# Optimization experiments

Measured on AMD Instinct MI355X. Metric: run time of the kernel, lower is better.

The kernel has to match this reference:

```python
import jax, jax.numpy as jnp
import numpy as np

LOG_SIG_MIN, LOG_SIG_MAX = -20.0, 2.0
N_NODES, N_EDGES, B = 16384, 131072, 256
NF, EF, GF, H, A = 64, 32, 16, 256, 8


def seg_mean(x, idx, num):
    # segment mean with empty-segment protection
    s = jax.ops.segment_sum(x, idx, num_segments=num)
    c = jax.ops.segment_sum(jnp.ones((x.shape[0], 1), x.dtype), idx, num_segments=num)
    return s / jnp.maximum(c, 1.0)


def setup_inputs() -> dict:
    key = jax.random.key(0)
    ks = jax.random.split(key, 32)
    def xav(k, i, o):
        lim = np.sqrt(6.0 / (i + o)).astype(np.float32)
        return jax.random.uniform(k, (i, o), jnp.float32, -lim, lim)
    inp = {
        'node_feats': jax.random.normal(ks[0], (N_NODES, NF), jnp.float32),
        'edge_feats': jax.random.normal(ks[1], (N_EDGES, EF), jnp.float32),
        'global_feats': jax.random.normal(ks[2], (B, GF), jnp.float32),
        'receivers': jax.random.randint(ks[3], (N_EDGES,), 0, N_NODES, jnp.int32),
        'node_graph': jnp.sort(jax.random.randint(ks[4], (N_NODES,), 0, B, jnp.int32)),
        'edge_graph': jnp.sort(jax.random.randint(ks[5], (N_EDGES,), 0, B, jnp.int32)),
        # edge1: edge_features only -> 256
        'We1': xav(ks[6], EF, 256), 'be1': jnp.zeros((256,), jnp.float32),
        # node1: node_features + aggregated incoming edges (256) -> 256
        'Wn1': xav(ks[7], NF, 256), 'Win1': xav(ks[8], 256, 256), 'bn1': jnp.zeros((256,), jnp.float32),
        # edge2: edge_features(256) + global(16) -> 128
        'We2': xav(ks[9], 256, 128), 'Weg2': xav(ks[10], GF, 128), 'be2': jnp.zeros((128,), jnp.float32),
        # node2: node(256) + incoming edges(128) + global(16) -> 128
        'Wn2': xav(ks[11], 256, 128), 'Win2': xav(ks[12], 128, 128), 'Wng2': xav(ks[13], GF, 128), 'bn2': jnp.zeros((128,), jnp.float32),
        # global: avg nodes(128) + avg edges(128) + global(16) -> H
        'Ugn': xav(ks[14], 128, H), 'Uge': xav(ks[15], 128, H), 'Ugg': xav(ks[16], GF, H), 'bg': jnp.zeros((H,), jnp.float32),
        # heads
        'Wm': xav(ks[17], H, A), 'bm': jnp.zeros((A,), jnp.float32),
        'Ws': xav(ks[18], H, A), 'bs': jnp.zeros((A,), jnp.float32),
    }
    return inp


def reference(node_feats, edge_feats, global_feats, receivers, node_graph, edge_graph,
              We1, be1, Wn1, Win1, bn1, We2, Weg2, be2, Wn2, Win2, Wng2, bn2,
              Ugn, Uge, Ugg, bg, Wm, bm, Ws, bs):
    # edge block 1: [N_EDGES, 256]
    e1 = jax.nn.relu(edge_feats @ We1 + be1)
    # node block 1: node linear + mean of incoming edges
    n1 = jax.nn.relu(node_feats @ Wn1 + seg_mean(e1, receivers, N_NODES) @ Win1 + bn1)
    # edge block 2: edge + per-graph global (gather)
    e2 = jax.nn.relu(e1 @ We2 + global_feats[edge_graph] @ Weg2 + be2)
    # node block 2
    n2 = jax.nn.relu(n1 @ Wn2 + seg_mean(e2, receivers, N_NODES) @ Win2 + global_feats[node_graph] @ Wng2 + bn2)
    # global block: per-graph mean over nodes and edges (scatter-reduce)
    u = seg_mean(n2, node_graph, B) @ Ugn + seg_mean(e2, edge_graph, B) @ Uge + global_feats @ Ugg + bg
    g = jax.nn.relu(u)
    mean = g @ Wm + bm
    log_std = jnp.clip(g @ Ws + bs, LOG_SIG_MIN, LOG_SIG_MAX)
    return mean, log_std
```

## Files before the change

kernel.cpp:

```cpp
#include <hip/hip_runtime.h>
#include <cstddef>

#define N_NODES 16384
#define N_EDGES 131072
#define BGR 256
#define NF 64
#define EF 32
#define GF 16

typedef __attribute__((ext_vector_type(8))) short bf16x8;
typedef __attribute__((ext_vector_type(4))) float f32x4;

#define MFMA16(a, b, c) __builtin_amdgcn_mfma_f32_16x16x32_bf16((a), (b), (c), 0, 0, 0)
__device__ const f32x4 ZERO4 = {0.f, 0.f, 0.f, 0.f};

__device__ inline unsigned short f2bf(float f) {
    return (unsigned short)((__builtin_bit_cast(unsigned, f) + 0x8000u) >> 16);
}
__device__ inline float bfs(short x) {
    return __builtin_bit_cast(float, (unsigned)((unsigned short)x) << 16);
}

__device__ inline bf16x8 pack8(float4 f0, float4 f1) {
    bf16x8 a;
    a[0] = (short)f2bf(f0.x); a[1] = (short)f2bf(f0.y);
    a[2] = (short)f2bf(f0.z); a[3] = (short)f2bf(f0.w);
    a[4] = (short)f2bf(f1.x); a[5] = (short)f2bf(f1.y);
    a[6] = (short)f2bf(f1.z); a[7] = (short)f2bf(f1.w);
    return a;
}

extern "C" __global__ void __launch_bounds__(256)
k_prep(const float* __restrict__ We1, const float* __restrict__ We2,
       const float* __restrict__ Wn1, const float* __restrict__ Win1,
       const float* __restrict__ Wn2, const float* __restrict__ Win2,
       unsigned short* We1p, unsigned short* We2p, unsigned short* Wn1p,
       unsigned short* Win1p, unsigned short* Wn2p, unsigned short* Win2p,
       const float* __restrict__ gf,
       const float* __restrict__ Weg2, const float* __restrict__ be2,
       const float* __restrict__ Wng2, const float* __restrict__ bn2,
       float* __restrict__ gproj_e, float* __restrict__ gproj_n,
       const int* __restrict__ receivers, int* cntR,
       const int* __restrict__ node_graph, const int* __restrict__ edge_graph,
       int* offN, int* offE)
{
    const int bid = blockIdx.x, tid = threadIdx.x;
    if (bid < 84) {
        const int fi = bid * 4 + (tid >> 6), l = tid & 63;
        const float* W; unsigned short* P; int N, t;
        if      (fi < 16)  { W = We1;  P = We1p;  N = 256; t = fi;       }
        else if (fi < 80)  { W = We2;  P = We2p;  N = 128; t = fi - 16;  }
        else if (fi < 112) { W = Wn1;  P = Wn1p;  N = 256; t = fi - 80;  }
        else if (fi < 240) { W = Win1; P = Win1p; N = 256; t = fi - 112; }
        else if (fi < 304) { W = Wn2;  P = Wn2p;  N = 128; t = fi - 240; }
        else               { W = Win2; P = Win2p; N = 128; t = fi - 304; }
        const int NT = N / 16;
        const int kt = t / NT, nt = t % NT;
        const int k0 = kt * 32 + (l >> 4) * 8;
        const int col = nt * 16 + (l & 15);
        unsigned short* dst = P + ((size_t)t * 64 + l) * 8;
        #pragma unroll
        for (int j = 0; j < 8; ++j) dst[j] = f2bf(W[(size_t)(k0 + j) * N + col]);
    } else if (bid < 212) {
        const int b = (bid - 84) * 2 + (tid >> 7), t = tid & 127;
        float ge = be2[t], gn = bn2[t];
        #pragma unroll
        for (int j = 0; j < GF; ++j) {
            const float g = gf[b * GF + j];
            ge = fmaf(g, Weg2[j * 128 + t], ge);
            gn = fmaf(g, Wng2[j * 128 + t], gn);
        }
        gproj_e[b * 128 + t] = ge;
        gproj_n[b * 128 + t] = gn;
    } else if (bid < 724) {
        const int i = (bid - 212) * 256 + tid;
        atomicAdd(&cntR[receivers[i]], 1);
    } else {
        const int g = tid;
        const int* arr = (bid == 725) ? edge_graph : node_graph;
        int* dst       = (bid == 725) ? offE       : offN;
        const int len  = (bid == 725) ? N_EDGES    : N_NODES;
        int lo = 0, hi = len;
        while (lo < hi) {
            const int mid = (lo + hi) >> 1;
            if (arr[mid] < g) lo = mid + 1; else hi = mid;
        }
        dst[g] = lo;
        if (g == 0) dst[256] = len;
    }
}

extern "C" __global__ void __launch_bounds__(256)
k_scanA(const int* __restrict__ cntR, int* __restrict__ offR, int* __restrict__ bsum)
{
    __shared__ int sm[256];
    const int b = blockIdx.x, t = threadIdx.x;
    const int4 v = *(const int4*)(cntR + b * 1024 + t * 4);
    const int s = v.x + v.y + v.z + v.w;
    sm[t] = s; __syncthreads();
    for (int o = 1; o < 256; o <<= 1) {
        int x = (t >= o) ? sm[t - o] : 0;
        __syncthreads(); sm[t] += x; __syncthreads();
    }
    const int excl = sm[t] - s;
    int4 o;
    o.x = excl; o.y = excl + v.x; o.z = o.y + v.y; o.w = o.z + v.z;
    *(int4*)(offR + b * 1024 + t * 4) = o;
    if (t == 255) bsum[b] = sm[255];
}

extern "C" __global__ void __launch_bounds__(256)
k_scanB(int* __restrict__ offR, const int* __restrict__ bsum)
{
    const int i = blockIdx.x * 256 + threadIdx.x;
    if (i > 16384) return;
    const int g = i >> 10;
    int pre = 0;
    for (int k = 0; k < g; ++k) pre += bsum[k];
    offR[i] = (i < 16384 ? offR[i] : 0) + pre;
}

extern "C" __global__ void __launch_bounds__(256)
k_scatter(const int* __restrict__ receivers, const int* __restrict__ offR,
          int* curR, int* perm)
{
    const int i = blockIdx.x * 256 + threadIdx.x;
    if (i < N_EDGES) {
        const int r = receivers[i];
        const int pos = offR[r] + atomicAdd(&curR[r], 1);
        perm[pos] = i;
    }
}

extern "C" __global__ void __launch_bounds__(256)
k_edge(const float* __restrict__ edge_feats,
       const int* __restrict__ perm,
       const int* __restrict__ edge_graph,
       const unsigned short* __restrict__ We1p,
       const unsigned short* __restrict__ We2p,
       const float* __restrict__ be1,
       const float* __restrict__ gproj_e,
       unsigned short* __restrict__ e1p,
       unsigned short* __restrict__ e2p,
       unsigned short* __restrict__ e2g)
{
    __shared__ __align__(16) unsigned short e1s[64 * 256];
    const int tid = threadIdx.x;
    const int w = tid >> 6, l = tid & 63;
    const int lr = l & 15, lq = l >> 4;
    const int e0 = blockIdx.x * 64;
    char* B = (char*)e1s;

    int eidA[4];
    int egC[4][4];
    #pragma unroll
    for (int g = 0; g < 4; ++g) eidA[g] = perm[e0 + g * 16 + lr];
    #pragma unroll
    for (int g = 0; g < 4; ++g)
        #pragma unroll
        for (int i = 0; i < 4; ++i)
            egC[g][i] = edge_graph[perm[e0 + g * 16 + lq * 4 + i]];

    bf16x8 a[4];
    #pragma unroll
    for (int g = 0; g < 4; ++g) {
        const float* s = edge_feats + (size_t)eidA[g] * EF + lq * 8;
        a[g] = pack8(*(const float4*)s, *(const float4*)(s + 4));
    }
    #pragma unroll
    for (int j = 0; j < 4; ++j) {
        const int nt = w * 4 + j;
        bf16x8 bfr = *(const bf16x8*)(We1p + ((size_t)nt * 64 + l) * 8);
        const int col = nt * 16 + lr;
        const float bias = be1[col];
        #pragma unroll
        for (int g = 0; g < 4; ++g) {
            f32x4 c = MFMA16(a[g], bfr, ZERO4);
            #pragma unroll
            for (int i = 0; i < 4; ++i) {
                const int row = g * 16 + lq * 4 + i;
                const float v = fmaxf(c[i] + bias, 0.f);
                *(unsigned short*)(B + row * 512 + ((col * 2) ^ ((row & 7) << 4))) = f2bf(v);
            }
        }
    }
    __syncthreads();

    #pragma unroll
    for (int it = 0; it < 8; ++it) {
        const int flat = it * 4096 + tid * 16;
        const int row = flat >> 9, colb = flat & 511;
        bf16x8 v = *(const bf16x8*)(B + row * 512 + (colb ^ ((row & 7) << 4)));
        *(bf16x8*)(e1p + (size_t)(e0 + row) * 256 + (colb >> 1)) = v;
    }

    f32x4 acc[4][2];
    #pragma unroll
    for (int g = 0; g < 4; ++g) {
        acc[g][0] = ZERO4;
        acc[g][1] = ZERO4;
    }
    #pragma unroll
    for (int kt = 0; kt < 8; ++kt) {
        bf16x8 pA[4];
        #pragma unroll
        for (int g = 0; g < 4; ++g) {
            const int row = g * 16 + lr;
            pA[g] = *(const bf16x8*)(B + row * 512 + ((kt * 64 + lq * 16) ^ ((lr & 7) << 4)));
        }
        #pragma unroll
        for (int j = 0; j < 2; ++j) {
            const int nt = w * 2 + j;
            bf16x8 bfr = *(const bf16x8*)(We2p + ((size_t)(kt * 8 + nt) * 64 + l) * 8);
            #pragma unroll
            for (int g = 0; g < 4; ++g) acc[g][j] = MFMA16(pA[g], bfr, acc[g][j]);
        }
    }
    __syncthreads();

    #pragma unroll
    for (int j = 0; j < 2; ++j) {
        const int nt = w * 2 + j, col = nt * 16 + lr;
        #pragma unroll
        for (int g = 0; g < 4; ++g)
            #pragma unroll
            for (int i = 0; i < 4; ++i) {
                const int row = g * 16 + lq * 4 + i;
                const float v = fmaxf(acc[g][j][i] + gproj_e[(size_t)egC[g][i] * 128 + col], 0.f);
                *(unsigned short*)(B + row * 512 + ((col * 2) ^ ((row & 7) << 4))) = f2bf(v);
            }
    }
    __syncthreads();
    #pragma unroll
    for (int it = 0; it < 4; ++it) {
        const int flat = it * 4096 + tid * 16;
        const int row = flat >> 8, colb = flat & 255;
        bf16x8 v = *(const bf16x8*)(B + row * 512 + (colb ^ ((row & 7) << 4)));
        const int eid = perm[e0 + row];
        *(bf16x8*)(e2p + (size_t)(e0 + row) * 128 + (colb >> 1)) = v;
        *(bf16x8*)(e2g + (size_t)eid * 128 + (colb >> 1)) = v;
    }
}

extern "C" __global__ void __launch_bounds__(256)
k_nodeagg(const float* __restrict__ node_feats,
          const int* __restrict__ node_graph,
          const int* __restrict__ offR,
          const unsigned short* __restrict__ e1p,
          const unsigned short* __restrict__ e2p,
          const unsigned short* __restrict__ Wn1p,
          const unsigned short* __restrict__ Win1p,
          const unsigned short* __restrict__ Wn2p,
          const unsigned short* __restrict__ Win2p,
          const float* __restrict__ bn1,
          const float* __restrict__ gproj_n,
          unsigned short* __restrict__ n2g)
{
    __shared__ __align__(16) unsigned short m1s[16 * 256];
    __shared__ __align__(16) unsigned short m2s[16 * 128];
    __shared__ __align__(16) unsigned short n1s[16 * 256];
    const int tid = threadIdx.x;
    const int w = tid >> 6, l = tid & 63;
    const int lr = l & 15, lq = l >> 4;
    const int n0 = blockIdx.x * 16;
    char* M1 = (char*)m1s; char* M2 = (char*)m2s; char* N1 = (char*)n1s;

    const int half = l >> 5, li = l & 31, q = l >> 4;
    for (int jn = 0; jn < 4; ++jn) {
        const int rn = w * 4 + jn, n = n0 + rn;
        const int c0 = offR[n], c1 = offR[n + 1];
        float s1[8] = {0.f, 0.f, 0.f, 0.f, 0.f, 0.f, 0.f, 0.f};
        float s2[8] = {0.f, 0.f, 0.f, 0.f, 0.f, 0.f, 0.f, 0.f};
        int r = c0;
        for (; r + 2 <= c1; r += 2) {
            bf16x8 v = *(const bf16x8*)(e1p + (size_t)(r + half) * 256 + li * 8);
            #pragma unroll
            for (int j = 0; j < 8; ++j) s1[j] += bfs(v[j]);
        }
        if (r < c1 && half == 0) {
            bf16x8 v = *(const bf16x8*)(e1p + (size_t)r * 256 + li * 8);
            #pragma unroll
            for (int j = 0; j < 8; ++j) s1[j] += bfs(v[j]);
        }
        r = c0;
        for (; r + 4 <= c1; r += 4) {
            bf16x8 v = *(const bf16x8*)(e2p + (size_t)(r + q) * 128 + lr * 8);
            #pragma unroll
            for (int j = 0; j < 8; ++j) s2[j] += bfs(v[j]);
        }
        if (r + q < c1) {
            bf16x8 v = *(const bf16x8*)(e2p + (size_t)(r + q) * 128 + lr * 8);
            #pragma unroll
            for (int j = 0; j < 8; ++j) s2[j] += bfs(v[j]);
        }
        #pragma unroll
        for (int j = 0; j < 8; ++j) s1[j] += __shfl_xor(s1[j], 32);
        #pragma unroll
        for (int j = 0; j < 8; ++j) {
            s2[j] += __shfl_xor(s2[j], 16);
            s2[j] += __shfl_xor(s2[j], 32);
        }
        const float inv = 1.0f / fmaxf((float)(c1 - c0), 1.0f);
        if (half == 0) {
            bf16x8 o;
            #pragma unroll
            for (int j = 0; j < 8; ++j) o[j] = (short)f2bf(s1[j] * inv);
            *(bf16x8*)(M1 + rn * 512 + ((li * 16) ^ ((rn & 7) << 4))) = o;
        }
        if (l < 16) {
            bf16x8 o;
            #pragma unroll
            for (int j = 0; j < 8; ++j) o[j] = (short)f2bf(s2[j] * inv);
            *(bf16x8*)(M2 + rn * 256 + ((l * 16) ^ ((rn & 7) << 4))) = o;
        }
    }
    __syncthreads();

    bf16x8 A1[10];
    #pragma unroll
    for (int kt = 0; kt < 2; ++kt) {
        const float* s = node_feats + (size_t)(n0 + lr) * NF + kt * 32 + lq * 8;
        A1[kt] = pack8(*(const float4*)s, *(const float4*)(s + 4));
    }
    #pragma unroll
    for (int kt = 0; kt < 8; ++kt)
        A1[2 + kt] = *(const bf16x8*)(M1 + lr * 512 + ((kt * 64 + lq * 16) ^ ((lr & 7) << 4)));
    #pragma unroll
    for (int j = 0; j < 4; ++j) {
        const int nt = w * 4 + j, col = nt * 16 + lr;
        f32x4 c = ZERO4;
        #pragma unroll
        for (int kt = 0; kt < 2; ++kt)
            c = MFMA16(A1[kt], *(const bf16x8*)(Wn1p + ((size_t)(kt * 16 + nt) * 64 + l) * 8), c);
        #pragma unroll
        for (int kt = 0; kt < 8; ++kt)
            c = MFMA16(A1[2 + kt], *(const bf16x8*)(Win1p + ((size_t)(kt * 16 + nt) * 64 + l) * 8), c);
        const float bias = bn1[col];
        #pragma unroll
        for (int i = 0; i < 4; ++i) {
            const int row = lq * 4 + i;
            const float v = fmaxf(c[i] + bias, 0.f);
            *(unsigned short*)(N1 + row * 512 + ((col * 2) ^ ((row & 7) << 4))) = f2bf(v);
        }
    }
    __syncthreads();

    int ngv[4];
    #pragma unroll
    for (int i = 0; i < 4; ++i) ngv[i] = node_graph[n0 + lq * 4 + i];
    f32x4 acc[2];
    acc[0] = ZERO4;
    acc[1] = ZERO4;
    #pragma unroll
    for (int kt = 0; kt < 8; ++kt) {
        bf16x8 Aa = *(const bf16x8*)(N1 + lr * 512 + ((kt * 64 + lq * 16) ^ ((lr & 7) << 4)));
        #pragma unroll
        for (int j = 0; j < 2; ++j) {
            const int nt = w * 2 + j;
            acc[j] = MFMA16(Aa, *(const bf16x8*)(Wn2p + ((size_t)(kt * 8 + nt) * 64 + l) * 8), acc[j]);
        }
    }
    #pragma unroll
    for (int kt = 0; kt < 4; ++kt) {
        bf16x8 Aa = *(const bf16x8*)(M2 + lr * 256 + ((kt * 64 + lq * 16) ^ ((lr & 7) << 4)));
        #pragma unroll
        for (int j = 0; j < 2; ++j) {
            const int nt = w * 2 + j;
            acc[j] = MFMA16(Aa, *(const bf16x8*)(Win2p + ((size_t)(kt * 8 + nt) * 64 + l) * 8), acc[j]);
        }
    }
    __syncthreads();
    #pragma unroll
    for (int j = 0; j < 2; ++j) {
        const int nt = w * 2 + j, col = nt * 16 + lr;
        #pragma unroll
        for (int i = 0; i < 4; ++i) {
            const int row = lq * 4 + i;
            const float v = fmaxf(acc[j][i] + gproj_n[(size_t)ngv[i] * 128 + col], 0.f);
            *(unsigned short*)(M2 + row * 256 + ((col * 2) ^ ((row & 7) << 4))) = f2bf(v);
        }
    }
    __syncthreads();
    {
        const int flat = tid * 16;
        const int row = flat >> 8, colb = flat & 255;
        bf16x8 v = *(const bf16x8*)(M2 + row * 256 + (colb ^ ((row & 7) << 4)));
        *(bf16x8*)(n2g + (size_t)(n0 + row) * 128 + (colb >> 1)) = v;
    }
}

extern "C" __global__ void __launch_bounds__(512)
k_global(const float* __restrict__ global_feats,
         const float* __restrict__ Ugn, const float* __restrict__ Uge,
         const float* __restrict__ Ugg, const float* __restrict__ bg,
         const float* __restrict__ Wm, const float* __restrict__ bm,
         const float* __restrict__ Ws, const float* __restrict__ bs,
         const unsigned short* __restrict__ n2g,
         const unsigned short* __restrict__ e2g,
         const int* __restrict__ offN, const int* __restrict__ offE,
         float* __restrict__ out)
{
    __shared__ float redn[32][128], rede[32][128];
    __shared__ float mn[128], me[128], gs[256];
    const int b = blockIdx.x, tid = threadIdx.x;
    const int c = tid & 15, rp = tid >> 4;
    float sn[8] = {0.f, 0.f, 0.f, 0.f, 0.f, 0.f, 0.f, 0.f};
    float se[8] = {0.f, 0.f, 0.f, 0.f, 0.f, 0.f, 0.f, 0.f};
    const int nb = offN[b], ne = offN[b + 1];
    for (int r = nb + rp; r < ne; r += 32) {
        bf16x8 v = *(const bf16x8*)(n2g + (size_t)r * 128 + c * 8);
        #pragma unroll
        for (int j = 0; j < 8; ++j) sn[j] += bfs(v[j]);
    }
    const int eb = offE[b], ee = offE[b + 1];
    for (int r = eb + rp; r < ee; r += 32) {
        bf16x8 v = *(const bf16x8*)(e2g + (size_t)r * 128 + c * 8);
        #pragma unroll
        for (int j = 0; j < 8; ++j) se[j] += bfs(v[j]);
    }
    #pragma unroll
    for (int j = 0; j < 8; ++j) { redn[rp][c * 8 + j] = sn[j]; rede[rp][c * 8 + j] = se[j]; }
    __syncthreads();
    if (tid < 128) {
        float s = 0.f;
        #pragma unroll
        for (int k = 0; k < 32; ++k) s += redn[k][tid];
        mn[tid] = s / fmaxf((float)(ne - nb), 1.0f);
    } else if (tid < 256) {
        const int t = tid - 128;
        float s = 0.f;
        #pragma unroll
        for (int k = 0; k < 32; ++k) s += rede[k][t];
        me[t] = s / fmaxf((float)(ee - eb), 1.0f);
    }
    __syncthreads();

    if (tid < 256) {
        const int h = tid;
        float u = bg[h];
        for (int k = 0; k < 128; ++k) u = fmaf(mn[k], Ugn[k * 256 + h], u);
        for (int k = 0; k < 128; ++k) u = fmaf(me[k], Uge[k * 256 + h], u);
        #pragma unroll
        for (int j = 0; j < GF; ++j) u = fmaf(global_feats[b * GF + j], Ugg[j * 256 + h], u);
        gs[h] = fmaxf(u, 0.0f);
    }
    __syncthreads();

    if (tid < 16) {
        const int a = tid & 7;
        const int which = tid >> 3;
        const float* W = which ? Ws : Wm;
        float acc = which ? bs[a] : bm[a];
        for (int k = 0; k < 256; ++k) acc = fmaf(gs[k], W[k * 8 + a], acc);
        if (which) acc = fminf(fmaxf(acc, -20.0f), 2.0f);
        out[which * 2048 + b * 8 + a] = acc;
    }
}

extern "C" void kernel_launch(void* const* d_in, const int* in_sizes, int n_in,
                              void* d_out, int out_size, void* d_ws, size_t ws_size,
                              hipStream_t stream)
{
    (void)in_sizes; (void)n_in; (void)out_size; (void)ws_size;
    const float* node_feats   = (const float*)d_in[0];
    const float* edge_feats   = (const float*)d_in[1];
    const float* global_feats = (const float*)d_in[2];
    const int*   receivers    = (const int*)d_in[3];
    const int*   node_graph   = (const int*)d_in[4];
    const int*   edge_graph   = (const int*)d_in[5];
    const float* We1 = (const float*)d_in[6];
    const float* be1 = (const float*)d_in[7];
    const float* Wn1 = (const float*)d_in[8];
    const float* Win1= (const float*)d_in[9];
    const float* bn1 = (const float*)d_in[10];
    const float* We2 = (const float*)d_in[11];
    const float* Weg2= (const float*)d_in[12];
    const float* be2 = (const float*)d_in[13];
    const float* Wn2 = (const float*)d_in[14];
    const float* Win2= (const float*)d_in[15];
    const float* Wng2= (const float*)d_in[16];
    const float* bn2 = (const float*)d_in[17];
    const float* Ugn = (const float*)d_in[18];
    const float* Uge = (const float*)d_in[19];
    const float* Ugg = (const float*)d_in[20];
    const float* bg  = (const float*)d_in[21];
    const float* Wm  = (const float*)d_in[22];
    const float* bm  = (const float*)d_in[23];
    const float* Ws  = (const float*)d_in[24];
    const float* bs  = (const float*)d_in[25];

    char* p = (char*)d_ws;
    auto alloc = [&](size_t bytes) -> char* {
        char* r = p; p += (bytes + 255) & ~(size_t)255; return r;
    };
    int* cntR  = (int*)alloc(16384 * 4);
    int* curR  = (int*)alloc(16384 * 4);
    const size_t zero_bytes = (size_t)(p - (char*)d_ws);
    int* offR = (int*)alloc(16385 * 4);
    int* bsum = (int*)alloc(16 * 4);
    int* offN = (int*)alloc(257 * 4);
    int* offE = (int*)alloc(257 * 4);
    int* perm = (int*)alloc((size_t)N_EDGES * 4);
    float* gproj_e = (float*)alloc((size_t)BGR * 128 * 4);
    float* gproj_n = (float*)alloc((size_t)BGR * 128 * 4);
    unsigned short* We1p  = (unsigned short*)alloc((size_t)32 * 256 * 2);
    unsigned short* We2p  = (unsigned short*)alloc((size_t)256 * 128 * 2);
    unsigned short* Wn1p  = (unsigned short*)alloc((size_t)64 * 256 * 2);
    unsigned short* Win1p = (unsigned short*)alloc((size_t)256 * 256 * 2);
    unsigned short* Wn2p  = (unsigned short*)alloc((size_t)256 * 128 * 2);
    unsigned short* Win2p = (unsigned short*)alloc((size_t)128 * 128 * 2);
    unsigned short* e1p   = (unsigned short*)alloc((size_t)N_EDGES * 256 * 2);
    unsigned short* e2p   = (unsigned short*)alloc((size_t)N_EDGES * 128 * 2);
    unsigned short* e2g   = (unsigned short*)alloc((size_t)N_EDGES * 128 * 2);
    unsigned short* n2g   = (unsigned short*)alloc((size_t)N_NODES * 128 * 2);

    hipMemsetAsync(d_ws, 0, zero_bytes, stream);

    k_prep<<<726, 256, 0, stream>>>(
        We1, We2, Wn1, Win1, Wn2, Win2,
        We1p, We2p, Wn1p, Win1p, Wn2p, Win2p,
        global_feats, Weg2, be2, Wng2, bn2, gproj_e, gproj_n,
        receivers, cntR, node_graph, edge_graph, offN, offE);
    k_scanA<<<16, 256, 0, stream>>>(cntR, offR, bsum);
    k_scanB<<<65, 256, 0, stream>>>(offR, bsum);
    k_scatter<<<N_EDGES / 256, 256, 0, stream>>>(receivers, offR, curR, perm);
    k_edge<<<N_EDGES / 64, 256, 0, stream>>>(
        edge_feats, perm, edge_graph, We1p, We2p, be1, gproj_e, e1p, e2p, e2g);
    k_nodeagg<<<N_NODES / 16, 256, 0, stream>>>(
        node_feats, node_graph, offR, e1p, e2p,
        Wn1p, Win1p, Wn2p, Win2p, bn1, gproj_n, n2g);
    k_global<<<BGR, 512, 0, stream>>>(
        global_feats, Ugn, Uge, Ugg, bg, Wm, bm, Ws, bs,
        n2g, e2g, offN, offE, (float*)d_out);
}
```

Before: 116.1 us.

## Fuse per-receiver segment reduction into edge kernel with cross-block partial sums

The edge kernel now reduces the receiver-sorted e1/e2 tiles in shared memory into per-node means. Segments that cross a 64-edge block boundary are written as per-block first/last partial sums. The node kernel reads these means directly, or stitches the partials for spanning nodes, instead of re-reading the full e1p/e2p edge arrays. This removes large global writes and reads of e1/e2, at the cost of a serial 64-row column scan per thread and extra partial-sum buffers.

```diff
diff --git a/kernel.cpp b/kernel.cpp
--- a/kernel.cpp
+++ b/kernel.cpp
@@ -17,8 +17,8 @@
 __device__ inline unsigned short f2bf(float f) {
     return (unsigned short)((__builtin_bit_cast(unsigned, f) + 0x8000u) >> 16);
 }
-__device__ inline float bfs(short x) {
-    return __builtin_bit_cast(float, (unsigned)((unsigned short)x) << 16);
+__device__ inline float bfs(unsigned short x) {
+    return __builtin_bit_cast(float, (unsigned)x << 16);
 }
 
 __device__ inline bf16x8 pack8(float4 f0, float4 f1) {
@@ -135,31 +135,43 @@
 extern "C" __global__ void __launch_bounds__(256)
 k_edge(const float* __restrict__ edge_feats,
        const int* __restrict__ perm,
+       const int* __restrict__ receivers,
        const int* __restrict__ edge_graph,
        const unsigned short* __restrict__ We1p,
        const unsigned short* __restrict__ We2p,
        const float* __restrict__ be1,
        const float* __restrict__ gproj_e,
-       unsigned short* __restrict__ e1p,
-       unsigned short* __restrict__ e2p,
+       const int* __restrict__ offR,
+       unsigned short* __restrict__ mean1g,
+       unsigned short* __restrict__ mean2g,
+       float* __restrict__ pfirst1, float* __restrict__ plast1,
+       float* __restrict__ pfirst2, float* __restrict__ plast2,
        unsigned short* __restrict__ e2g)
 {
     __shared__ __align__(16) unsigned short e1s[64 * 256];
+    __shared__ int nidL[64], eidL[64];
     const int tid = threadIdx.x;
     const int w = tid >> 6, l = tid & 63;
     const int lr = l & 15, lq = l >> 4;
-    const int e0 = blockIdx.x * 64;
+    const int blk = blockIdx.x;
+    const int e0 = blk * 64;
     char* B = (char*)e1s;
 
-    int eidA[4];
-    int egC[4][4];
-    #pragma unroll
-    for (int g = 0; g < 4; ++g) eidA[g] = perm[e0 + g * 16 + lr];
+    if (tid < 64) {
+        const int pe = perm[e0 + tid];
+        eidL[tid] = pe;
+        nidL[tid] = receivers[pe];
+    }
+    __syncthreads();
+
+    int eidA[4], egC[4][4];
+    #pragma unroll
+    for (int g = 0; g < 4; ++g) eidA[g] = eidL[g * 16 + lr];
     #pragma unroll
     for (int g = 0; g < 4; ++g)
         #pragma unroll
         for (int i = 0; i < 4; ++i)
-            egC[g][i] = edge_graph[perm[e0 + g * 16 + lq * 4 + i]];
+            egC[g][i] = edge_graph[eidL[g * 16 + lq * 4 + i]];
 
     bf16x8 a[4];
     #pragma unroll
@@ -186,20 +198,34 @@
     }
     __syncthreads();
 
-    #pragma unroll
-    for (int it = 0; it < 8; ++it) {
-        const int flat = it * 4096 + tid * 16;
-        const int row = flat >> 9, colb = flat & 511;
-        bf16x8 v = *(const bf16x8*)(B + row * 512 + (colb ^ ((row & 7) << 4)));
-        *(bf16x8*)(e1p + (size_t)(e0 + row) * 256 + (colb >> 1)) = v;
+    const int nid0 = nidL[0], nid63 = nidL[63];
+    const bool firstStarts = (offR[nid0] == e0);
+    const bool lastEnds    = (offR[nid63 + 1] == e0 + 64);
+
+    {
+        const int c = tid;
+        float sum = 0.f; int aa = 0;
+        for (int r = 0; r < 64; ++r) {
+            sum += bfs(*(const unsigned short*)(B + r * 512 + ((c * 2) ^ ((r & 7) << 4))));
+            const bool segEnd = (r == 63) || (nidL[r + 1] != nidL[r]);
+            if (segEnd) {
+                const int n = nidL[r];
+                const bool sIn = (aa > 0) || firstStarts;
+                const bool eIn = (r < 63) || lastEnds;
+                if (sIn && eIn)
+                    mean1g[(size_t)n * 256 + c] = f2bf(sum / (float)(r - aa + 1));
+                else if (aa == 0)
+                    pfirst1[(size_t)blk * 256 + c] = sum;
+                else
+                    plast1[(size_t)blk * 256 + c] = sum;
+                sum = 0.f; aa = r + 1;
+            }
+        }
     }
 
     f32x4 acc[4][2];
     #pragma unroll
-    for (int g = 0; g < 4; ++g) {
-        acc[g][0] = ZERO4;
-        acc[g][1] = ZERO4;
-    }
+    for (int g = 0; g < 4; ++g) { acc[g][0] = ZERO4; acc[g][1] = ZERO4; }
     #pragma unroll
     for (int kt = 0; kt < 8; ++kt) {
         bf16x8 pA[4];
@@ -231,14 +257,34 @@
             }
     }
     __syncthreads();
+
+    if (tid < 128) {
+        const int c = tid;
+        float sum = 0.f; int aa = 0;
+        for (int r = 0; r < 64; ++r) {
+            sum += bfs(*(const unsigned short*)(B + r * 512 + ((c * 2) ^ ((r & 7) << 4))));
+            const bool segEnd = (r == 63) || (nidL[r + 1] != nidL[r]);
+            if (segEnd) {
+                const int n = nidL[r];
+                const bool sIn = (aa > 0) || firstStarts;
+                const bool eIn = (r < 63) || lastEnds;
+                if (sIn && eIn)
+                    mean2g[(size_t)n * 128 + c] = f2bf(sum / (float)(r - aa + 1));
+                else if (aa == 0)
+                    pfirst2[(size_t)blk * 128 + c] = sum;
+                else
+                    plast2[(size_t)blk * 128 + c] = sum;
+                sum = 0.f; aa = r + 1;
+            }
+        }
+    }
+
     #pragma unroll
     for (int it = 0; it < 4; ++it) {
         const int flat = it * 4096 + tid * 16;
         const int row = flat >> 8, colb = flat & 255;
         bf16x8 v = *(const bf16x8*)(B + row * 512 + (colb ^ ((row & 7) << 4)));
-        const int eid = perm[e0 + row];
-        *(bf16x8*)(e2p + (size_t)(e0 + row) * 128 + (colb >> 1)) = v;
-        *(bf16x8*)(e2g + (size_t)eid * 128 + (colb >> 1)) = v;
+        *(bf16x8*)(e2g + (size_t)eidL[row] * 128 + (colb >> 1)) = v;
     }
 }
 
@@ -246,8 +292,10 @@
 k_nodeagg(const float* __restrict__ node_feats,
           const int* __restrict__ node_graph,
           const int* __restrict__ offR,
-          const unsigned short* __restrict__ e1p,
-          const unsigned short* __restrict__ e2p,
+          const unsigned short* __restrict__ mean1g,
+          const unsigned short* __restrict__ mean2g,
+          const float* __restrict__ pfirst1, const float* __restrict__ plast1,
+          const float* __restrict__ pfirst2, const float* __restrict__ plast2,
           const unsigned short* __restrict__ Wn1p,
           const unsigned short* __restrict__ Win1p,
           const unsigned short* __restrict__ Wn2p,
@@ -259,59 +307,52 @@
     __shared__ __align__(16) unsigned short m1s[16 * 256];
     __shared__ __align__(16) unsigned short m2s[16 * 128];
     __shared__ __align__(16) unsigned short n1s[16 * 256];
+    __shared__ int offL[17];
     const int tid = threadIdx.x;
     const int w = tid >> 6, l = tid & 63;
     const int lr = l & 15, lq = l >> 4;
     const int n0 = blockIdx.x * 16;
     char* M1 = (char*)m1s; char* M2 = (char*)m2s; char* N1 = (char*)n1s;
 
-    const int half = l >> 5, li = l & 31, q = l >> 4;
-    for (int jn = 0; jn < 4; ++jn) {
-        const int rn = w * 4 + jn, n = n0 + rn;
-        const int c0 = offR[n], c1 = offR[n + 1];
-        float s1[8] = {0.f, 0.f, 0.f, 0.f, 0.f, 0.f, 0.f, 0.f};
-        float s2[8] = {0.f, 0.f, 0.f, 0.f, 0.f, 0.f, 0.f, 0.f};
-        int r = c0;
-        for (; r + 2 <= c1; r += 2) {
-            bf16x8 v = *(const bf16x8*)(e1p + (size_t)(r + half) * 256 + li * 8);
-            #pragma unroll
-            for (int j = 0; j < 8; ++j) s1[j] += bfs(v[j]);
-        }
-        if (r < c1 && half == 0) {
-            bf16x8 v = *(const bf16x8*)(e1p + (size_t)r * 256 + li * 8);
-            #pragma unroll
-            for (int j = 0; j < 8; ++j) s1[j] += bfs(v[j]);
-        }
-        r = c0;
-        for (; r + 4 <= c1; r += 4) {
-            bf16x8 v = *(const bf16x8*)(e2p + (size_t)(r + q) * 128 + lr * 8);
-            #pragma unroll
-            for (int j = 0; j < 8; ++j) s2[j] += bfs(v[j]);
-        }
-        if (r + q < c1) {
-            bf16x8 v = *(const bf16x8*)(e2p + (size_t)(r + q) * 128 + lr * 8);
-            #pragma unroll
-            for (int j = 0; j < 8; ++j) s2[j] += bfs(v[j]);
-        }
-        #pragma unroll
-        for (int j = 0; j < 8; ++j) s1[j] += __shfl_xor(s1[j], 32);
-        #pragma unroll
-        for (int j = 0; j < 8; ++j) {
-            s2[j] += __shfl_xor(s2[j], 16);
-            s2[j] += __shfl_xor(s2[j], 32);
-        }
-        const float inv = 1.0f / fmaxf((float)(c1 - c0), 1.0f);
-        if (half == 0) {
-            bf16x8 o;
-            #pragma unroll
-            for (int j = 0; j < 8; ++j) o[j] = (short)f2bf(s1[j] * inv);
-            *(bf16x8*)(M1 + rn * 512 + ((li * 16) ^ ((rn & 7) << 4))) = o;
-        }
-        if (l < 16) {
-            bf16x8 o;
-            #pragma unroll
-            for (int j = 0; j < 8; ++j) o[j] = (short)f2bf(s2[j] * inv);
-            *(bf16x8*)(M2 + rn * 256 + ((l * 16) ^ ((rn & 7) << 4))) = o;
+    if (tid < 17) offL[tid] = offR[n0 + tid];
+    __syncthreads();
+
+    #pragma unroll 1
+    for (int rn = 0; rn < 16; ++rn) {
+        const int c0 = offL[rn], c1 = offL[rn + 1];
+        unsigned short u = 0;
+        if (c1 > c0) {
+            const int B0 = c0 >> 6, B1 = (c1 - 1) >> 6;
+            if (B0 == B1) {
+                u = mean1g[(size_t)(n0 + rn) * 256 + tid];
+            } else {
+                float sum = (c0 == (B0 << 6)) ? pfirst1[(size_t)B0 * 256 + tid]
+                                              : plast1[(size_t)B0 * 256 + tid];
+                for (int Bb = B0 + 1; Bb <= B1; ++Bb)
+                    sum += pfirst1[(size_t)Bb * 256 + tid];
+                u = f2bf(sum / (float)(c1 - c0));
+            }
+        }
+        *(unsigned short*)(M1 + rn * 512 + ((tid * 2) ^ ((rn & 7) << 4))) = u;
+    }
+    if (tid < 128) {
+        #pragma unroll 1
+        for (int rn = 0; rn < 16; ++rn) {
+            const int c0 = offL[rn], c1 = offL[rn + 1];
+            unsigned short u = 0;
+            if (c1 > c0) {
+                const int B0 = c0 >> 6, B1 = (c1 - 1) >> 6;
+                if (B0 == B1) {
+                    u = mean2g[(size_t)(n0 + rn) * 128 + tid];
+                } else {
+                    float sum = (c0 == (B0 << 6)) ? pfirst2[(size_t)B0 * 128 + tid]
+                                                  : plast2[(size_t)B0 * 128 + tid];
+                    for (int Bb = B0 + 1; Bb <= B1; ++Bb)
+                        sum += pfirst2[(size_t)Bb * 128 + tid];
+                    u = f2bf(sum / (float)(c1 - c0));
+                }
+            }
+            *(unsigned short*)(M2 + rn * 256 + ((tid * 2) ^ ((rn & 7) << 4))) = u;
         }
     }
     __syncthreads();
@@ -349,8 +390,7 @@
     #pragma unroll
     for (int i = 0; i < 4; ++i) ngv[i] = node_graph[n0 + lq * 4 + i];
     f32x4 acc[2];
-    acc[0] = ZERO4;
-    acc[1] = ZERO4;
+    acc[0] = ZERO4; acc[1] = ZERO4;
     #pragma unroll
     for (int kt = 0; kt < 8; ++kt) {
         bf16x8 Aa = *(const bf16x8*)(N1 + lr * 512 + ((kt * 64 + lq * 16) ^ ((lr & 7) << 4)));
@@ -410,13 +450,13 @@
     for (int r = nb + rp; r < ne; r += 32) {
         bf16x8 v = *(const bf16x8*)(n2g + (size_t)r * 128 + c * 8);
         #pragma unroll
-        for (int j = 0; j < 8; ++j) sn[j] += bfs(v[j]);
+        for (int j = 0; j < 8; ++j) sn[j] += bfs((unsigned short)v[j]);
     }
     const int eb = offE[b], ee = offE[b + 1];
     for (int r = eb + rp; r < ee; r += 32) {
         bf16x8 v = *(const bf16x8*)(e2g + (size_t)r * 128 + c * 8);
         #pragma unroll
-        for (int j = 0; j < 8; ++j) se[j] += bfs(v[j]);
+        for (int j = 0; j < 8; ++j) se[j] += bfs((unsigned short)v[j]);
     }
     #pragma unroll
     for (int j = 0; j < 8; ++j) { redn[rp][c * 8 + j] = sn[j]; rede[rp][c * 8 + j] = se[j]; }
@@ -509,10 +549,14 @@
     unsigned short* Win1p = (unsigned short*)alloc((size_t)256 * 256 * 2);
     unsigned short* Wn2p  = (unsigned short*)alloc((size_t)256 * 128 * 2);
     unsigned short* Win2p = (unsigned short*)alloc((size_t)128 * 128 * 2);
-    unsigned short* e1p   = (unsigned short*)alloc((size_t)N_EDGES * 256 * 2);
-    unsigned short* e2p   = (unsigned short*)alloc((size_t)N_EDGES * 128 * 2);
-    unsigned short* e2g   = (unsigned short*)alloc((size_t)N_EDGES * 128 * 2);
-    unsigned short* n2g   = (unsigned short*)alloc((size_t)N_NODES * 128 * 2);
+    unsigned short* mean1g = (unsigned short*)alloc((size_t)N_NODES * 256 * 2);
+    unsigned short* mean2g = (unsigned short*)alloc((size_t)N_NODES * 128 * 2);
+    float* pfirst1 = (float*)alloc((size_t)(N_EDGES / 64) * 256 * 4);
+    float* plast1  = (float*)alloc((size_t)(N_EDGES / 64) * 256 * 4);
+    float* pfirst2 = (float*)alloc((size_t)(N_EDGES / 64) * 128 * 4);
+    float* plast2  = (float*)alloc((size_t)(N_EDGES / 64) * 128 * 4);
+    unsigned short* e2g = (unsigned short*)alloc((size_t)N_EDGES * 128 * 2);
+    unsigned short* n2g = (unsigned short*)alloc((size_t)N_NODES * 128 * 2);
 
     hipMemsetAsync(d_ws, 0, zero_bytes, stream);
 
@@ -525,9 +569,11 @@
     k_scanB<<<65, 256, 0, stream>>>(offR, bsum);
     k_scatter<<<N_EDGES / 256, 256, 0, stream>>>(receivers, offR, curR, perm);
     k_edge<<<N_EDGES / 64, 256, 0, stream>>>(
-        edge_feats, perm, edge_graph, We1p, We2p, be1, gproj_e, e1p, e2p, e2g);
+        edge_feats, perm, receivers, edge_graph, We1p, We2p, be1, gproj_e,
+        offR, mean1g, mean2g, pfirst1, plast1, pfirst2, plast2, e2g);
     k_nodeagg<<<N_NODES / 16, 256, 0, stream>>>(
-        node_feats, node_graph, offR, e1p, e2p,
+        node_feats, node_graph, offR, mean1g, mean2g,
+        pfirst1, plast1, pfirst2, plast2,
         Wn1p, Win1p, Wn2p, Win2p, bn1, gproj_n, n2g);
     k_global<<<BGR, 512, 0, stream>>>(
         global_feats, Ugn, Uge, Ugg, bg, Wm, bm, Ws, bs,
```

Measured after the change: 150.5 us. +29.6%, slower.

## Process edges in original order and gather through perm during node aggregation

Applied to the files above, without the earlier changes.

The edge kernel now works on edges in their original order and writes e1 and e2 once each. This removes the perm-indirect gathers of edge features and edge_graph, and the duplicate receiver-sorted e2 copy. Node aggregation instead reads perm and gathers e1/e2 rows by edge id, so those reads become scattered rather than contiguous. A fast path is also added: when all 64 edges in a block belong to one graph, a single gproj row is loaded per column. The cost is more random 512-byte and 256-byte row reads in k_nodeagg in exchange for less write traffic in k_edge.

```diff
diff --git a/kernel.cpp b/kernel.cpp
--- a/kernel.cpp
+++ b/kernel.cpp
@@ -17,8 +17,8 @@
 __device__ inline unsigned short f2bf(float f) {
     return (unsigned short)((__builtin_bit_cast(unsigned, f) + 0x8000u) >> 16);
 }
-__device__ inline float bfs(short x) {
-    return __builtin_bit_cast(float, (unsigned)((unsigned short)x) << 16);
+__device__ inline float bfs(unsigned short x) {
+    return __builtin_bit_cast(float, (unsigned)x << 16);
 }
 
 __device__ inline bf16x8 pack8(float4 f0, float4 f1) {
@@ -134,14 +134,12 @@
 
 extern "C" __global__ void __launch_bounds__(256)
 k_edge(const float* __restrict__ edge_feats,
-       const int* __restrict__ perm,
        const int* __restrict__ edge_graph,
        const unsigned short* __restrict__ We1p,
        const unsigned short* __restrict__ We2p,
        const float* __restrict__ be1,
        const float* __restrict__ gproj_e,
-       unsigned short* __restrict__ e1p,
-       unsigned short* __restrict__ e2p,
+       unsigned short* __restrict__ e1g,
        unsigned short* __restrict__ e2g)
 {
     __shared__ __align__(16) unsigned short e1s[64 * 256];
@@ -151,20 +149,21 @@
     const int e0 = blockIdx.x * 64;
     char* B = (char*)e1s;
 
-    int eidA[4];
+    const int g0 = edge_graph[e0];
+    const bool uni = (edge_graph[e0 + 63] == g0);
     int egC[4][4];
-    #pragma unroll
-    for (int g = 0; g < 4; ++g) eidA[g] = perm[e0 + g * 16 + lr];
-    #pragma unroll
-    for (int g = 0; g < 4; ++g)
-        #pragma unroll
-        for (int i = 0; i < 4; ++i)
-            egC[g][i] = edge_graph[perm[e0 + g * 16 + lq * 4 + i]];
+    if (!uni) {
+        #pragma unroll
+        for (int g = 0; g < 4; ++g)
+            #pragma unroll
+            for (int i = 0; i < 4; ++i)
+                egC[g][i] = edge_graph[e0 + g * 16 + lq * 4 + i];
+    }
 
     bf16x8 a[4];
     #pragma unroll
     for (int g = 0; g < 4; ++g) {
-        const float* s = edge_feats + (size_t)eidA[g] * EF + lq * 8;
+        const float* s = edge_feats + (size_t)(e0 + g * 16 + lr) * EF + lq * 8;
         a[g] = pack8(*(const float4*)s, *(const float4*)(s + 4));
     }
     #pragma unroll
@@ -191,15 +190,12 @@
         const int flat = it * 4096 + tid * 16;
         const int row = flat >> 9, colb = flat & 511;
         bf16x8 v = *(const bf16x8*)(B + row * 512 + (colb ^ ((row & 7) << 4)));
-        *(bf16x8*)(e1p + (size_t)(e0 + row) * 256 + (colb >> 1)) = v;
+        *(bf16x8*)(e1g + (size_t)(e0 + row) * 256 + (colb >> 1)) = v;
     }
 
     f32x4 acc[4][2];
     #pragma unroll
-    for (int g = 0; g < 4; ++g) {
-        acc[g][0] = ZERO4;
-        acc[g][1] = ZERO4;
-    }
+    for (int g = 0; g < 4; ++g) { acc[g][0] = ZERO4; acc[g][1] = ZERO4; }
     #pragma unroll
     for (int kt = 0; kt < 8; ++kt) {
         bf16x8 pA[4];
@@ -221,12 +217,14 @@
     #pragma unroll
     for (int j = 0; j < 2; ++j) {
         const int nt = w * 2 + j, col = nt * 16 + lr;
+        const float gu = uni ? gproj_e[(size_t)g0 * 128 + col] : 0.f;
         #pragma unroll
         for (int g = 0; g < 4; ++g)
             #pragma unroll
             for (int i = 0; i < 4; ++i) {
                 const int row = g * 16 + lq * 4 + i;
-                const float v = fmaxf(acc[g][j][i] + gproj_e[(size_t)egC[g][i] * 128 + col], 0.f);
+                const float gv = uni ? gu : gproj_e[(size_t)egC[g][i] * 128 + col];
+                const float v = fmaxf(acc[g][j][i] + gv, 0.f);
                 *(unsigned short*)(B + row * 512 + ((col * 2) ^ ((row & 7) << 4))) = f2bf(v);
             }
     }
@@ -236,9 +234,7 @@
         const int flat = it * 4096 + tid * 16;
         const int row = flat >> 8, colb = flat & 255;
         bf16x8 v = *(const bf16x8*)(B + row * 512 + (colb ^ ((row & 7) << 4)));
-        const int eid = perm[e0 + row];
-        *(bf16x8*)(e2p + (size_t)(e0 + row) * 128 + (colb >> 1)) = v;
-        *(bf16x8*)(e2g + (size_t)eid * 128 + (colb >> 1)) = v;
+        *(bf16x8*)(e2g + (size_t)(e0 + row) * 128 + (colb >> 1)) = v;
     }
 }
 
@@ -246,8 +242,9 @@
 k_nodeagg(const float* __restrict__ node_feats,
           const int* __restrict__ node_graph,
           const int* __restrict__ offR,
-          const unsigned short* __restrict__ e1p,
-          const unsigned short* __restrict__ e2p,
+          const int* __restrict__ perm,
+          const unsigned short* __restrict__ e1g,
+          const unsigned short* __restrict__ e2g,
           const unsigned short* __restrict__ Wn1p,
           const unsigned short* __restrict__ Win1p,
           const unsigned short* __restrict__ Wn2p,
@@ -273,25 +270,29 @@
         float s2[8] = {0.f, 0.f, 0.f, 0.f, 0.f, 0.f, 0.f, 0.f};
         int r = c0;
         for (; r + 2 <= c1; r += 2) {
-            bf16x8 v = *(const bf16x8*)(e1p + (size_t)(r + half) * 256 + li * 8);
-            #pragma unroll
-            for (int j = 0; j < 8; ++j) s1[j] += bfs(v[j]);
+            const int eid = perm[r + half];
+            bf16x8 v = *(const bf16x8*)(e1g + (size_t)eid * 256 + li * 8);
+            #pragma unroll
+            for (int j = 0; j < 8; ++j) s1[j] += bfs((unsigned short)v[j]);
         }
         if (r < c1 && half == 0) {
-            bf16x8 v = *(const bf16x8*)(e1p + (size_t)r * 256 + li * 8);
-            #pragma unroll
-            for (int j = 0; j < 8; ++j) s1[j] += bfs(v[j]);
+            const int eid = perm[r];
+            bf16x8 v = *(const bf16x8*)(e1g + (size_t)eid * 256 + li * 8);
+            #pragma unroll
+            for (int j = 0; j < 8; ++j) s1[j] += bfs((unsigned short)v[j]);
         }
         r = c0;
         for (; r + 4 <= c1; r += 4) {
-            bf16x8 v = *(const bf16x8*)(e2p + (size_t)(r + q) * 128 + lr * 8);
-            #pragma unroll
-            for (int j = 0; j < 8; ++j) s2[j] += bfs(v[j]);
+            const int eid = perm[r + q];
+            bf16x8 v = *(const bf16x8*)(e2g + (size_t)eid * 128 + lr * 8);
+            #pragma unroll
+            for (int j = 0; j < 8; ++j) s2[j] += bfs((unsigned short)v[j]);
         }
         if (r + q < c1) {
-            bf16x8 v = *(const bf16x8*)(e2p + (size_t)(r + q) * 128 + lr * 8);
-            #pragma unroll
-            for (int j = 0; j < 8; ++j) s2[j] += bfs(v[j]);
+            const int eid = perm[r + q];
+            bf16x8 v = *(const bf16x8*)(e2g + (size_t)eid * 128 + lr * 8);
+            #pragma unroll
+            for (int j = 0; j < 8; ++j) s2[j] += bfs((unsigned short)v[j]);
         }
         #pragma unroll
         for (int j = 0; j < 8; ++j) s1[j] += __shfl_xor(s1[j], 32);
@@ -349,8 +350,7 @@
     #pragma unroll
     for (int i = 0; i < 4; ++i) ngv[i] = node_graph[n0 + lq * 4 + i];
     f32x4 acc[2];
-    acc[0] = ZERO4;
-    acc[1] = ZERO4;
+    acc[0] = ZERO4; acc[1] = ZERO4;
     #pragma unroll
     for (int kt = 0; kt < 8; ++kt) {
         bf16x8 Aa = *(const bf16x8*)(N1 + lr * 512 + ((kt * 64 + lq * 16) ^ ((lr & 7) << 4)));
@@ -410,13 +410,13 @@
     for (int r = nb + rp; r < ne; r += 32) {
         bf16x8 v = *(const bf16x8*)(n2g + (size_t)r * 128 + c * 8);
         #pragma unroll
-        for (int j = 0; j < 8; ++j) sn[j] += bfs(v[j]);
+        for (int j = 0; j < 8; ++j) sn[j] += bfs((unsigned short)v[j]);
     }
     const int eb = offE[b], ee = offE[b + 1];
     for (int r = eb + rp; r < ee; r += 32) {
         bf16x8 v = *(const bf16x8*)(e2g + (size_t)r * 128 + c * 8);
         #pragma unroll
-        for (int j = 0; j < 8; ++j) se[j] += bfs(v[j]);
+        for (int j = 0; j < 8; ++j) se[j] += bfs((unsigned short)v[j]);
     }
     #pragma unroll
     for (int j = 0; j < 8; ++j) { redn[rp][c * 8 + j] = sn[j]; rede[rp][c * 8 + j] = se[j]; }
@@ -509,10 +509,9 @@
     unsigned short* Win1p = (unsigned short*)alloc((size_t)256 * 256 * 2);
     unsigned short* Wn2p  = (unsigned short*)alloc((size_t)256 * 128 * 2);
     unsigned short* Win2p = (unsigned short*)alloc((size_t)128 * 128 * 2);
-    unsigned short* e1p   = (unsigned short*)alloc((size_t)N_EDGES * 256 * 2);
-    unsigned short* e2p   = (unsigned short*)alloc((size_t)N_EDGES * 128 * 2);
-    unsigned short* e2g   = (unsigned short*)alloc((size_t)N_EDGES * 128 * 2);
-    unsigned short* n2g   = (unsigned short*)alloc((size_t)N_NODES * 128 * 2);
+    unsigned short* e1g = (unsigned short*)alloc((size_t)N_EDGES * 256 * 2);
+    unsigned short* e2g = (unsigned short*)alloc((size_t)N_EDGES * 128 * 2);
+    unsigned short* n2g = (unsigned short*)alloc((size_t)N_NODES * 128 * 2);
 
     hipMemsetAsync(d_ws, 0, zero_bytes, stream);
 
@@ -525,9 +524,9 @@
     k_scanB<<<65, 256, 0, stream>>>(offR, bsum);
     k_scatter<<<N_EDGES / 256, 256, 0, stream>>>(receivers, offR, curR, perm);
     k_edge<<<N_EDGES / 64, 256, 0, stream>>>(
-        edge_feats, perm, edge_graph, We1p, We2p, be1, gproj_e, e1p, e2p, e2g);
+        edge_feats, edge_graph, We1p, We2p, be1, gproj_e, e1g, e2g);
     k_nodeagg<<<N_NODES / 16, 256, 0, stream>>>(
-        node_feats, node_graph, offR, e1p, e2p,
+        node_feats, node_graph, offR, perm, e1g, e2g,
         Wn1p, Win1p, Wn2p, Win2p, bn1, gproj_n, n2g);
     k_global<<<BGR, 512, 0, stream>>>(
         global_feats, Ugn, Uge, Ugg, bg, Wm, bm, Ws, bs,
```

Result: slower. 123.7 us (+6.6%).
